# Performance work log

Measured on AMD Instinct MI355X. Metric: run time of the kernel, lower is better.

Reference implementation:

```python
import jax, jax.numpy as jnp
import numpy as np

# --- dims (match init_kwargs) ---
H = 2048      # hidden_dim
NH = 16       # num_heads
QL = 1536     # q_latent_dim
KVL = 512     # kv_latent_dim
QR = 64       # q_rope_dim (== k_rope_dim)
QN = 128      # q_nope_dim
KR = 64       # k_rope_dim
KN = 128      # k_nope_dim
VD = 128      # v_dim
B, S = 1, 2048
BASE = 10000.0
EPS = 1e-6


def rms_norm(x, w, eps=EPS):
    xf = x.astype(jnp.float32)
    var = jnp.mean(xf * xf, axis=-1, keepdims=True)
    return w * (xf * jax.lax.rsqrt(var + eps)).astype(x.dtype)


def rope_cos_sin(seq_len, dim, base=BASE):
    inv_freq = 1.0 / (base ** (jnp.arange(0, dim, 2, dtype=jnp.float32) / dim))
    t = jnp.arange(seq_len, dtype=jnp.float32)
    freqs = jnp.outer(t, inv_freq)
    emb = jnp.concatenate([freqs, freqs], axis=-1)  # [S, dim]
    return jnp.cos(emb), jnp.sin(emb)


def rotate_half(x):
    d = x.shape[-1] // 2
    return jnp.concatenate([-x[..., d:], x[..., :d]], axis=-1)


def apply_rotary_pos_emb(q, k, cos, sin, position_ids):
    # cos/sin: [S, d]; position_ids: [B, S] -> [B, 1, S, d]
    cos = cos[position_ids][:, None]
    sin = sin[position_ids][:, None]

    def interleave(x):  # matches view(b,h,s,d//2,2).transpose(4,3).reshape
        b, h, s, d = x.shape
        return x.reshape(b, h, s, d // 2, 2).transpose(0, 1, 2, 4, 3).reshape(b, h, s, d)

    q = interleave(q)
    k = interleave(k)
    return q * cos + rotate_half(q) * sin, k * cos + rotate_half(k) * sin


def setup_inputs() -> dict:
    key = jax.random.key(0)
    ks = jax.random.split(key, 8)
    sc = 0.02
    hidden_states = jax.random.normal(ks[0], (B, S, H), dtype=jnp.float32)
    position_ids = jnp.broadcast_to(jnp.arange(S, dtype=jnp.int32), (B, S))
    attn_mask = jnp.tril(jnp.ones((S, S), dtype=jnp.int32))[None, None]  # causal, [1,1,S,S]
    return {
        "hidden_states": hidden_states,
        "position_ids": position_ids,
        "attn_mask": attn_mask,
        "q_down_w": jax.random.normal(ks[1], (QL, H), jnp.float32) * sc,
        "kv_down_w": jax.random.normal(ks[2], (KVL + KR, H), jnp.float32) * sc,
        "q_up_w": jax.random.normal(ks[3], (NH * (QN + QR), QL), jnp.float32) * sc,
        "k_up_w": jax.random.normal(ks[4], (NH * (KN + VD), KVL), jnp.float32) * sc,
        "o_w": jax.random.normal(ks[5], (H, NH * VD), jnp.float32) * sc,
        "q_norm_w": jnp.ones((QL,), jnp.float32),
        "kv_norm_w": jnp.ones((KVL + KR,), jnp.float32),
    }


def reference(hidden_states, position_ids, attn_mask, q_down_w, kv_down_w,
              q_up_w, k_up_w, o_w, q_norm_w, kv_norm_w):
    bsz, seq_len, _ = hidden_states.shape

    # --- query path: down-proj -> RMSNorm -> up-proj ---
    latent_cq = rms_norm(hidden_states @ q_down_w.T, q_norm_w)        # [B,S,QL]
    q = latent_cq @ q_up_w.T                                          # [B,S,NH*(QN+QR)]
    q = q.reshape(bsz, seq_len, NH, QN + QR).transpose(0, 2, 1, 3)    # [B,NH,S,QN+QR]
    q_nope, q_pe = q[..., :QN], q[..., QN:]

    # --- kv path: down-proj -> RMSNorm -> split latent / shared k_pe ---
    compressed_kv = rms_norm(hidden_states @ kv_down_w.T, kv_norm_w)  # [B,S,KVL+KR]
    latent_ckv, k_pe = compressed_kv[..., :KVL], compressed_kv[..., KVL:]
    kv = latent_ckv @ k_up_w.T                                        # [B,S,NH*(KN+VD)]
    kv = kv.reshape(bsz, seq_len, NH, KN + VD).transpose(0, 2, 1, 3)  # [B,NH,S,KN+VD]
    k_nope, value = kv[..., :KN], kv[..., KN:]

    # --- partial RoPE on rotary sub-dims ---
    cos, sin = rope_cos_sin(seq_len, QR)
    k_pe = k_pe[:, None]                                              # [B,1,S,KR] shared across heads
    q_rope, k_rope = apply_rotary_pos_emb(q_pe, k_pe, cos, sin, position_ids)
    k_rope = jnp.broadcast_to(k_rope, (bsz, NH, seq_len, KR))

    query = jnp.concatenate([q_rope, q_nope], axis=-1)                # [B,NH,S,QR+QN]
    key = jnp.concatenate([k_rope, k_nope], axis=-1)                  # [B,NH,S,KR+KN]

    # --- explicit attention (no 1/sqrt(d) scale, matching the source) ---
    attn_weights = jnp.einsum('bhqd,bhkd->bhqk', query, key)
    attn_weights = jnp.where(attn_mask == 0, -jnp.inf, attn_weights)
    attn_weights = jax.nn.softmax(attn_weights, axis=-1)
    attn_output = jnp.einsum('bhqk,bhkd->bhqd', attn_weights, value)
    attn_output = attn_output.transpose(0, 2, 1, 3).reshape(bsz, seq_len, NH * VD)
    attn_output = attn_output @ o_w.T                                 # [B,S,H]
    return attn_weights, attn_output
```

## Files before the change

### kernel.cpp

```cpp
#include <hip/hip_runtime.h>
#include <cstdint>
#include <cmath>

typedef _Float16 f16;
using f16x8 = __attribute__((ext_vector_type(8))) _Float16;
using f16x4 = __attribute__((ext_vector_type(4))) _Float16;
using f32x4 = __attribute__((ext_vector_type(4))) float;

#define NHEAD 16
#define SEQ   2048
#define KS    2
#define KSS   4
#define NEG_INF -3.0e38f

static __device__ __forceinline__ f32x4 mfma16(f16x8 a, f16x8 b, f32x4 c) {
    return __builtin_amdgcn_mfma_f32_16x16x32_f16(a, b, c, 0, 0, 0);
}

static __device__ __forceinline__ void gload16(const void* gp, void* lp) {
    __builtin_amdgcn_global_load_lds(
        (const __attribute__((address_space(1))) unsigned int*)gp,
        (__attribute__((address_space(3))) unsigned int*)lp, 16, 0, 0);
}

__global__ __launch_bounds__(256) void k_cvt_all(
    const float* __restrict__ hsrc, const float* __restrict__ qdw, const float* __restrict__ kvdw,
    const float* __restrict__ quw, const float* __restrict__ kuw, const float* __restrict__ ow,
    f16* __restrict__ h16, f16* __restrict__ dw16, f16* __restrict__ quw16,
    f16* __restrict__ kuw16, f16* __restrict__ ow16, float* __restrict__ cs)
{
    constexpr int C1 = 1048576;
    constexpr int C2 = C1 + 786432;
    constexpr int C3 = C2 + 327680;
    constexpr int C4 = C3 + 1179648;
    constexpr int C5 = C4 + 524288;
    constexpr int C6 = C5 + 1048576;
    int chunk = blockIdx.x * 256 + threadIdx.x;
    if (chunk >= C6) {
        int idx = chunk - C6;
        if (idx < 65536) {
            int t = idx >> 5, j = idx & 31;
            float invf = (float)pow(10000.0, -(double)j / 32.0);
            float ang  = (float)t * invf;
            cs[t * 64 + j]      = (float)cos((double)ang);
            cs[t * 64 + 32 + j] = (float)sin((double)ang);
        }
        return;
    }
    const float* src; f16* dst; int off; int nvalid;
    if (chunk < C1)      { src = hsrc; dst = h16;  off = chunk;      nvalid = 4194304; }
    else if (chunk < C2) { src = qdw;  dst = dw16; off = chunk - C1; nvalid = 3145728; }
    else if (chunk < C3) { src = kvdw; dst = dw16 + 3145728; off = chunk - C2; nvalid = 1179648; }
    else if (chunk < C4) { src = quw;  dst = quw16; off = chunk - C3; nvalid = 4718592; }
    else if (chunk < C5) { src = kuw;  dst = kuw16; off = chunk - C4; nvalid = 2097152; }
    else                 { src = ow;   dst = ow16;  off = chunk - C5; nvalid = 4194304; }
    int i = off * 4;
    f16x4 o;
#pragma unroll
    for (int k = 0; k < 4; k++) {
        int idx = i + k;
        float v = (idx < nvalid) ? src[idx] : 0.f;
        o[k] = (f16)v;
    }
    *(f16x4*)&dst[i] = o;
}

template <typename OutT, bool NT>
static __device__ __forceinline__ void gemm_body(const f16* __restrict__ A, const f16* __restrict__ B,
                                                 OutT* __restrict__ C, int K, int ldc,
                                                 int m0, int n0, int k0, int k1,
                                                 f16* __restrict__ lds)
{
    const int tid  = threadIdx.x;
    const int lane = tid & 63;
    const int wv   = tid >> 6;
    const int l15  = lane & 15;
    const int lg   = lane >> 4;
    const int wm   = (wv >> 1) * 64;
    const int wn   = (wv & 1) * 64;

    f32x4 acc[4][4] = {};

    f16* As = lds;
    f16* Bs = lds + 8192;

    const int srow = tid >> 3;
    const int g    = (tid & 7) ^ (srow & 7);
    const f16* ap = &A[(size_t)(m0 + srow) * K + g * 8];
    const f16* bp = &B[(size_t)(n0 + srow) * K + g * 8];
    const int ldst = wv * 512;

    for (int kt = k0; kt < k1; kt += 64) {
        __syncthreads();
#pragma unroll
        for (int p = 0; p < 4; p++) {
            gload16(ap + (size_t)(p * 32) * K + kt, As + p * 2048 + ldst);
            gload16(bp + (size_t)(p * 32) * K + kt, Bs + p * 2048 + ldst);
        }
        __syncthreads();
#pragma unroll
        for (int ki = 0; ki < 2; ki++) {
            f16x8 af[4], bf[4];
#pragma unroll
            for (int i = 0; i < 4; i++) {
                const int ar = wm + i * 16 + l15;
                af[i] = *(const f16x8*)&As[ar * 64 + (((ki * 4 + lg) ^ (ar & 7)) << 3)];
            }
#pragma unroll
            for (int i = 0; i < 4; i++) {
                const int br = wn + i * 16 + l15;
                bf[i] = *(const f16x8*)&Bs[br * 64 + (((ki * 4 + lg) ^ (br & 7)) << 3)];
            }
#pragma unroll
            for (int i = 0; i < 4; i++)
#pragma unroll
                for (int j = 0; j < 4; j++)
                    acc[i][j] = mfma16(af[i], bf[j], acc[i][j]);
        }
    }
#pragma unroll
    for (int i = 0; i < 4; i++) {
#pragma unroll
        for (int j = 0; j < 4; j++) {
            const int row = m0 + wm + i * 16 + lg * 4;
            const int col = n0 + wn + j * 16 + l15;
#pragma unroll
            for (int r = 0; r < 4; r++) {
                if constexpr (NT)
                    __builtin_nontemporal_store((OutT)acc[i][j][r], &C[(size_t)(row + r) * ldc + col]);
                else
                    C[(size_t)(row + r) * ldc + col] = (OutT)acc[i][j][r];
            }
        }
    }
}

template <typename OutT, bool NT, int SPLITK>
__global__ __launch_bounds__(256) void k_gemm(const f16* __restrict__ A, const f16* __restrict__ B,
                                              OutT* __restrict__ C, int K, int ldc, size_t zstride)
{
    __shared__ __align__(16) f16 lds[16384];
    const int ks   = (SPLITK > 1) ? (int)blockIdx.z : 0;
    const int ksub = K / SPLITK;
    gemm_body<OutT, NT>(A, B, C + (size_t)ks * zstride, K, ldc,
                        blockIdx.y * 128, blockIdx.x * 128, ks * ksub, ks * ksub + ksub, lds);
}

__global__ __launch_bounds__(256) void k_up_fused(const f16* __restrict__ cq, const f16* __restrict__ quw,
                                                  f16* __restrict__ q_all,
                                                  const f16* __restrict__ lat, const f16* __restrict__ kuw,
                                                  f16* __restrict__ kv_all)
{
    __shared__ __align__(16) f16 lds[16384];
    if (blockIdx.x < 24)
        gemm_body<f16, false>(cq, quw, q_all, 1536, 3072,
                              blockIdx.y * 128, blockIdx.x * 128, 0, 1536, lds);
    else
        gemm_body<f16, false>(lat, kuw, kv_all, 512, 4096,
                              blockIdx.y * 128, (blockIdx.x - 24) * 128, 0, 512, lds);
}

__global__ __launch_bounds__(256) void k_add2f(const float* __restrict__ p, float* __restrict__ out)
{
    size_t i = ((size_t)blockIdx.x * 256 + threadIdx.x) * 4;
    f32x4 a = *(const f32x4*)&p[i];
    f32x4 b = *(const f32x4*)&p[(size_t)2048 * 2048 + i];
    __builtin_nontemporal_store(a + b, (f32x4*)&out[i]);
}

__global__ __launch_bounds__(256) void k_rms_both(const float* __restrict__ P0, const float* __restrict__ P1,
                                                  const float* __restrict__ wq, const float* __restrict__ wkv,
                                                  f16* __restrict__ cq, f16* __restrict__ lat,
                                                  f16* __restrict__ kro, const float* __restrict__ cs)
{
    const int row = blockIdx.x, tid = threadIdx.x;
    const float* a = &P0[(size_t)row * 2176];
    const float* b = &P1[(size_t)row * 2176];
    float ssq = 0.f, ssk = 0.f;
    for (int c = tid; c < 1536; c += 256) { float v = a[c] + b[c]; ssq += v * v; }
    for (int c = 1536 + tid; c < 2112; c += 256) { float v = a[c] + b[c]; ssk += v * v; }
#pragma unroll
    for (int off = 32; off > 0; off >>= 1) {
        ssq += __shfl_xor(ssq, off);
        ssk += __shfl_xor(ssk, off);
    }
    __shared__ float part[4][2];
    if ((tid & 63) == 0) { part[tid >> 6][0] = ssq; part[tid >> 6][1] = ssk; }
    __syncthreads();
    float totq = part[0][0] + part[1][0] + part[2][0] + part[3][0];
    float totk = part[0][1] + part[1][1] + part[2][1] + part[3][1];
    float scq = 1.f / sqrtf(totq / 1536.f + 1e-6f);
    float sck = 1.f / sqrtf(totk / 576.f + 1e-6f);
    for (int c = tid; c < 1536; c += 256)
        cq[(size_t)row * 1536 + c] = (f16)(wq[c] * (a[c] + b[c]) * scq);
    for (int c = tid; c < 512; c += 256)
        lat[(size_t)row * 512 + c] = (f16)(wkv[c] * (a[1536 + c] + b[1536 + c]) * sck);
    if (tid < 32) {
        int j = tid;
        float va = wkv[512 + 2 * j] * (a[2048 + 2 * j] + b[2048 + 2 * j]) * sck;
        float vb = wkv[512 + 2 * j + 1] * (a[2048 + 2 * j + 1] + b[2048 + 2 * j + 1]) * sck;
        float cv = cs[row * 64 + j], sv = cs[row * 64 + 32 + j];
        kro[row * 64 + j]      = (f16)(va * cv - vb * sv);
        kro[row * 64 + 32 + j] = (f16)(vb * cv + va * sv);
    }
}

__global__ __launch_bounds__(256) void k_asm_all(const f16* __restrict__ q_all, const float* __restrict__ cs,
                                                 f16* __restrict__ Qf,
                                                 const f16* __restrict__ kv_all,
                                                 f16* __restrict__ Knope,
                                                 f16* __restrict__ Vt)
{
    __shared__ __align__(16) f16 Vs[128][136];
    const int tid = threadIdx.x;

    if (blockIdx.x < 3072) {
        const int gid = blockIdx.x * 256 + tid;
        const int p   = gid % 24;
        const int rowi = gid / 24;
        const int h = rowi >> 11, s = rowi & 2047;
        const f16* qrow = &q_all[(size_t)s * 3072 + h * 192];
        f16x8 o;
        if (p < 8) {
            const int pp = (p < 4) ? p : (p - 4);
            f16x8 la = *(const f16x8*)&qrow[128 + 16 * pp];
            f16x8 lb = *(const f16x8*)&qrow[136 + 16 * pp];
            const float* cb = &cs[s * 64 + 8 * pp];
#pragma unroll
            for (int e = 0; e < 8; e++) {
                float av = (float)((e < 4) ? la[2 * e] : lb[2 * e - 8]);
                float bv = (float)((e < 4) ? la[2 * e + 1] : lb[2 * e - 7]);
                float cv = cb[e], sv = cb[32 + e];
                o[e] = (f16)((p < 4) ? (av * cv - bv * sv) : (bv * cv + av * sv));
            }
        } else {
            o = *(const f16x8*)&qrow[8 * p - 64];
        }
        *(f16x8*)&Qf[((size_t)h * SEQ + s) * 192 + 8 * p] = o;
        return;
    }

    const int b  = blockIdx.x - 3072;
    const int s0 = (b & 15) * 128;
    const int h  = b >> 4;
#pragma unroll
    for (int i = 0; i < 16; i++) {
        const int c = tid + 256 * i;
        const int s_loc = c >> 5;
        const int g = c & 31;
        f16x8 v = *(const f16x8*)&kv_all[(size_t)(s0 + s_loc) * 4096 + h * 256 + g * 8];
        if (g < 16) {
            *(f16x8*)&Knope[((size_t)h * 2048 + s0 + s_loc) * 128 + g * 8] = v;
        } else {
            const int d0 = (g - 16) * 8;
#pragma unroll
            for (int k = 0; k < 8; k++) Vs[d0 + k][s_loc] = v[k];
        }
    }
    __syncthreads();
#pragma unroll
    for (int i = 0; i < 8; i++) {
        const int c = tid + 256 * i;
        const int d = c >> 4;
        const int gs = c & 15;
        f16x8 v = *(const f16x8*)&Vs[d][gs * 8];
        *(f16x8*)&Vt[((size_t)h * 128 + d) * 2048 + s0 + gs * 8] = v;
    }
}

__global__ __launch_bounds__(256) void k_stats(
    const f16* __restrict__ Qf, const f16* __restrict__ Krope, const f16* __restrict__ Knope,
    float* __restrict__ mlpart)
{
    const int h  = blockIdx.z;
    const int ks = blockIdx.y;
    const int qt = blockIdx.x;
    const int q0 = qt * 64;
    const int tid = threadIdx.x;
    const int lane = tid & 63;
    const int wv = tid >> 6;
    const int l15 = lane & 15;
    const int lg  = lane >> 4;
    const int rowb = q0 + wv * 16;

    __shared__ __align__(16) f16 Ks_[64][200];

    float m[4], l[4];
#pragma unroll
    for (int r = 0; r < 4; r++) { m[r] = NEG_INF; l[r] = 0.f; }

    if (ks <= qt) {
        f16x8 qf[6];
        {
            const f16* qbase = &Qf[((size_t)h * SEQ + rowb + l15) * 192];
#pragma unroll
            for (int kf = 0; kf < 6; kf++)
                qf[kf] = *(const f16x8*)&qbase[kf * 32 + lg * 8];
        }
        const int srow = tid >> 2;
        const int sp4  = tid & 3;
        const f32x4 vzero = {0.f, 0.f, 0.f, 0.f};

        for (int t = ks; t <= qt; t += KSS) {
            const int c0 = t * 64;
            __syncthreads();
#pragma unroll
            for (int i = 0; i < 6; i++) {
                const int p = sp4 + 4 * i;
                f16x8 v;
                if (p < 8) v = *(const f16x8*)&Krope[(size_t)(c0 + srow) * 64 + p * 8];
                else       v = *(const f16x8*)&Knope[((size_t)h * SEQ + c0 + srow) * 128 + (p - 8) * 8];
                *(f16x8*)&Ks_[srow][p * 8] = v;
            }
            __syncthreads();

            f32x4 s[4];
#pragma unroll
            for (int ni = 0; ni < 4; ni++) {
                s[ni] = vzero;
                const f16* kp = &Ks_[ni * 16 + l15][0];
#pragma unroll
                for (int kf = 0; kf < 6; kf++)
                    s[ni] = mfma16(qf[kf], *(const f16x8*)&kp[kf * 32 + lg * 8], s[ni]);
            }

            float vmax[4] = {NEG_INF, NEG_INF, NEG_INF, NEG_INF};
#pragma unroll
            for (int ni = 0; ni < 4; ni++) {
                const int col = c0 + ni * 16 + l15;
#pragma unroll
                for (int r = 0; r < 4; r++) {
                    const int row = rowb + lg * 4 + r;
                    float v = (col <= row) ? s[ni][r] : NEG_INF;
                    s[ni][r] = v;
                    vmax[r] = fmaxf(vmax[r], v);
                }
            }
#pragma unroll
            for (int off = 1; off < 16; off <<= 1)
#pragma unroll
                for (int r = 0; r < 4; r++)
                    vmax[r] = fmaxf(vmax[r], __shfl_xor(vmax[r], off));
#pragma unroll
            for (int r = 0; r < 4; r++) {
                const float nm = fmaxf(m[r], vmax[r]);
                float es = 0.f;
#pragma unroll
                for (int ni = 0; ni < 4; ni++) es += expf(s[ni][r] - nm);
#pragma unroll
                for (int off = 1; off < 16; off <<= 1) es += __shfl_xor(es, off);
                l[r] = l[r] * expf(m[r] - nm) + es;
                m[r] = nm;
            }
        }
    }

    if (l15 == 0) {
#pragma unroll
        for (int r = 0; r < 4; r++) {
            const int rin = wv * 16 + lg * 4 + r;
            float* mp = &mlpart[((((size_t)h * 32 + qt) * KSS + ks) * 64 + rin) * 2];
            mp[0] = m[r];
            mp[1] = l[r];
        }
    }
}

__global__ __launch_bounds__(256) void k_pv(
    const f16* __restrict__ Qf, const f16* __restrict__ Krope, const f16* __restrict__ Knope,
    const f16* __restrict__ Vt, const float* __restrict__ mlpart,
    float* __restrict__ attnw,
    f16* __restrict__ Opart)
{
    const int h  = blockIdx.z;
    const int ks = blockIdx.y;
    const int qt = blockIdx.x;
    const int q0 = qt * 64;
    const int tid = threadIdx.x;
    const int lane = tid & 63;
    const int wv = tid >> 6;
    const int l15 = lane & 15;
    const int lg  = lane >> 4;
    const int rowb = q0 + wv * 16;

    __shared__ __align__(16) f16 Ks_[64][200];
    __shared__ __align__(16) f16 Vs[128][72];
    __shared__ __align__(16) f16 Plds[4][16][72];

    f16x8 qf[6];
    {
        const f16* qbase = &Qf[((size_t)h * SEQ + rowb + l15) * 192];
#pragma unroll
        for (int kf = 0; kf < 6; kf++)
            qf[kf] = *(const f16x8*)&qbase[kf * 32 + lg * 8];
    }

    float mr[4], rlr[4];
    {
        const float* base = &mlpart[(((size_t)h * 32 + qt) * KSS) * 64 * 2];
#pragma unroll
        for (int r = 0; r < 4; r++) {
            const int rin = wv * 16 + lg * 4 + r;
            float mm = NEG_INF, mk[KSS], lk[KSS];
#pragma unroll
            for (int k2 = 0; k2 < KSS; k2++) {
                mk[k2] = base[(k2 * 64 + rin) * 2];
                lk[k2] = base[(k2 * 64 + rin) * 2 + 1];
                mm = fmaxf(mm, mk[k2]);
            }
            float ll = 0.f;
#pragma unroll
            for (int k2 = 0; k2 < KSS; k2++) ll += lk[k2] * expf(mk[k2] - mm);
            mr[r]  = mm;
            rlr[r] = 1.f / ll;
        }
    }

    f32x4 o[8] = {};
    const f32x4 vzero = {0.f, 0.f, 0.f, 0.f};
    const int srow = tid >> 2;
    const int sp4  = tid & 3;

    for (int t = ks; t <= qt; t += KS) {
        const int c0 = t * 64;
        __syncthreads();
#pragma unroll
        for (int i = 0; i < 6; i++) {
            const int p = sp4 + 4 * i;
            f16x8 v;
            if (p < 8) v = *(const f16x8*)&Krope[(size_t)(c0 + srow) * 64 + p * 8];
            else       v = *(const f16x8*)&Knope[((size_t)h * SEQ + c0 + srow) * 128 + (p - 8) * 8];
            *(f16x8*)&Ks_[srow][p * 8] = v;
        }
#pragma unroll
        for (int i = 0; i < 4; i++) {
            const int c = tid + 256 * i;
            const int d = c >> 3, x = c & 7;
            *(f16x8*)&Vs[d][x * 8] = *(const f16x8*)&Vt[((size_t)h * 128 + d) * SEQ + c0 + x * 8];
        }
        __syncthreads();

        f32x4 s[4];
#pragma unroll
        for (int ni = 0; ni < 4; ni++) {
            s[ni] = vzero;
            const f16* kp = &Ks_[ni * 16 + l15][0];
#pragma unroll
            for (int kf = 0; kf < 6; kf++)
                s[ni] = mfma16(qf[kf], *(const f16x8*)&kp[kf * 32 + lg * 8], s[ni]);
        }

#pragma unroll
        for (int ni = 0; ni < 4; ni++) {
            const int col = c0 + ni * 16 + l15;
#pragma unroll
            for (int r = 0; r < 4; r++) {
                const int row = rowb + lg * 4 + r;
                float p = (col <= row) ? expf(s[ni][r] - mr[r]) * rlr[r] : 0.f;
                __builtin_nontemporal_store(p, &attnw[((size_t)h * SEQ + row) * SEQ + col]);
                Plds[wv][lg * 4 + r][ni * 16 + l15] = (f16)p;
            }
        }
        asm volatile("" ::: "memory");

        f16x8 pa0 = *(const f16x8*)&Plds[wv][l15][lg * 8];
        f16x8 pa1 = *(const f16x8*)&Plds[wv][l15][32 + lg * 8];
#pragma unroll
        for (int nd = 0; nd < 8; nd++) {
            const f16* vp = &Vs[nd * 16 + l15][lg * 8];
            o[nd] = mfma16(pa0, *(const f16x8*)&vp[0],  o[nd]);
            o[nd] = mfma16(pa1, *(const f16x8*)&vp[32], o[nd]);
        }
    }

#pragma unroll
    for (int nd = 0; nd < 8; nd++)
#pragma unroll
        for (int r = 0; r < 4; r++) {
            const int row = rowb + lg * 4 + r;
            Opart[((size_t)ks * SEQ + row) * 2048 + h * 128 + nd * 16 + l15] = (f16)o[nd][r];
        }

    if (ks == KS - 1) {
        const int cstart = q0 + 64;
        const int zc = SEQ - cstart;
        if (zc > 0) {
            const int nchunk = zc >> 2;
            for (int i = tid; i < 64 * nchunk; i += 256) {
                const int r  = i / nchunk;
                const int cc = (i - r * nchunk) << 2;
                __builtin_nontemporal_store(vzero,
                    (f32x4*)&attnw[((size_t)h * SEQ + q0 + r) * SEQ + cstart + cc]);
            }
        }
    }
}

__global__ __launch_bounds__(256) void k_ocomb(const f16* __restrict__ Opart, f16* __restrict__ Ohead)
{
    size_t i = ((size_t)blockIdx.x * 256 + threadIdx.x) * 8;
    f16x8 a = *(const f16x8*)&Opart[i];
    f16x8 b = *(const f16x8*)&Opart[(size_t)SEQ * 2048 + i];
    f16x8 o;
#pragma unroll
    for (int k = 0; k < 8; k++) o[k] = (f16)((float)a[k] + (float)b[k]);
    *(f16x8*)&Ohead[i] = o;
}

extern "C" void kernel_launch(void* const* d_in, const int* in_sizes, int n_in,
                              void* d_out, int out_size, void* d_ws, size_t ws_size,
                              hipStream_t stream)
{
    (void)in_sizes; (void)n_in; (void)out_size; (void)ws_size;
    const float* hidden    = (const float*)d_in[0];
    const float* q_down_w  = (const float*)d_in[3];
    const float* kv_down_w = (const float*)d_in[4];
    const float* q_up_w    = (const float*)d_in[5];
    const float* k_up_w    = (const float*)d_in[6];
    const float* o_w       = (const float*)d_in[7];
    const float* q_norm_w  = (const float*)d_in[8];
    const float* kv_norm_w = (const float*)d_in[9];

    float* attnw = (float*)d_out;
    float* outp  = attnw + (size_t)NHEAD * SEQ * SEQ;

    char* wp = (char*)d_ws;
    auto aws = [&](size_t bytes) { void* p = (void*)wp; wp += (bytes + 255) & ~(size_t)255; return p; };
    f16*  ow16  = (f16*)aws((size_t)2048 * 2048 * 2);
    f16*  Ohead = (f16*)aws((size_t)2048 * 2048 * 2);
    f16*  Qf    = (f16*)aws((size_t)16 * 2048 * 192 * 2);
    f16*  Knope = (f16*)aws((size_t)16 * 2048 * 128 * 2);
    f16*  Vt    = (f16*)aws((size_t)16 * 128 * 2048 * 2);
    f16*  Krope = (f16*)aws((size_t)2048 * 64 * 2);
    float* cs   = (float*)aws((size_t)2048 * 64 * 4);
    float* mlpart = (float*)aws((size_t)16 * 32 * KSS * 64 * 2 * 4);
    f16*  Opart   = (f16*)aws((size_t)KS * 2048 * 2048 * 2);
    float* opp    = (float*)Qf;

    char* sp = (char*)d_out;
    auto aso = [&](size_t bytes) { void* p = (void*)sp; sp += (bytes + 255) & ~(size_t)255; return p; };
    f16*  h16      = (f16*)aso((size_t)2048 * 2048 * 2);
    f16*  dw16     = (f16*)aso((size_t)2176 * 2048 * 2);
    f16*  quw16    = (f16*)aso((size_t)3072 * 1536 * 2);
    f16*  kuw16    = (f16*)aso((size_t)4096 * 512 * 2);
    float* down_part = (float*)aso((size_t)2 * 2048 * 2176 * 4);
    f16*  cq16     = (f16*)aso((size_t)2048 * 1536 * 2);
    f16*  latent16 = (f16*)aso((size_t)2048 * 512 * 2);
    f16*  q_all    = (f16*)aso((size_t)2048 * 3072 * 2);
    f16*  kv_all   = (f16*)aso((size_t)2048 * 4096 * 2);

    k_cvt_all<<<dim3(19456), dim3(256), 0, stream>>>(
        hidden, q_down_w, kv_down_w, q_up_w, k_up_w, o_w,
        h16, dw16, quw16, kuw16, ow16, cs);

    k_gemm<float, false, 2><<<dim3(17, 16, 2), dim3(256), 0, stream>>>(
        h16, dw16, down_part, 2048, 2176, (size_t)2048 * 2176);

    k_rms_both<<<dim3(2048), dim3(256), 0, stream>>>(
        down_part, down_part + (size_t)2048 * 2176, q_norm_w, kv_norm_w,
        cq16, latent16, Krope, cs);

    k_up_fused<<<dim3(56, 16), dim3(256), 0, stream>>>(cq16, quw16, q_all, latent16, kuw16, kv_all);

    k_asm_all<<<dim3(3072 + 256), dim3(256), 0, stream>>>(q_all, cs, Qf, kv_all, Knope, Vt);

    k_stats<<<dim3(32, KSS, 16), dim3(256), 0, stream>>>(Qf, Krope, Knope, mlpart);
    k_pv<<<dim3(32, KS, 16), dim3(256), 0, stream>>>(Qf, Krope, Knope, Vt, mlpart, attnw, Opart);
    k_ocomb<<<dim3(2048), dim3(256), 0, stream>>>(Opart, Ohead);

    k_gemm<float, false, 2><<<dim3(16, 16, 2), dim3(256), 0, stream>>>(
        Ohead, ow16, opp, 2048, 2048, (size_t)2048 * 2048);
    k_add2f<<<dim3(4096), dim3(256), 0, stream>>>(opp, outp);
}
```

Measured before the change: 376.7 us.

## Use 128-row query tiles with 512-thread blocks in attention kernels

The stats and PV attention kernels now handle 128 query rows per block with 8 waves instead of 64 rows with 4 waves. Each staged K/V tile in shared memory is therefore reused by twice as many query rows. Heads 8 and up process query tiles in reverse order to even out causal load across blocks. Waves whose rows lie entirely above a key tile skip the compute, and in PV they write zeros to those attention-weight entries. The cost is fewer blocks in the grid and some waves idling on diagonal tiles.

```diff
diff --git a/kernel.cpp b/kernel.cpp
--- a/kernel.cpp
+++ b/kernel.cpp
@@ -268,14 +268,14 @@
     }
 }
 
-__global__ __launch_bounds__(256) void k_stats(
+__global__ __launch_bounds__(512) void k_stats(
     const f16* __restrict__ Qf, const f16* __restrict__ Krope, const f16* __restrict__ Knope,
     float* __restrict__ mlpart)
 {
     const int h  = blockIdx.z;
     const int ks = blockIdx.y;
-    const int qt = blockIdx.x;
-    const int q0 = qt * 64;
+    const int qt = (h >= 8) ? (15 - (int)blockIdx.x) : (int)blockIdx.x;
+    const int q0 = qt * 128;
     const int tid = threadIdx.x;
     const int lane = tid & 63;
     const int wv = tid >> 6;
@@ -289,7 +289,8 @@
 #pragma unroll
     for (int r = 0; r < 4; r++) { m[r] = NEG_INF; l[r] = 0.f; }
 
-    if (ks <= qt) {
+    const int ntiles = 2 * qt + 2;
+    if (ks < ntiles) {
         f16x8 qf[6];
         {
             const f16* qbase = &Qf[((size_t)h * SEQ + rowb + l15) * 192];
@@ -297,22 +298,24 @@
             for (int kf = 0; kf < 6; kf++)
                 qf[kf] = *(const f16x8*)&qbase[kf * 32 + lg * 8];
         }
-        const int srow = tid >> 2;
-        const int sp4  = tid & 3;
+        const int srow = tid >> 3;
+        const int sp8  = tid & 7;
         const f32x4 vzero = {0.f, 0.f, 0.f, 0.f};
 
-        for (int t = ks; t <= qt; t += KSS) {
+        for (int t = ks; t < ntiles; t += KSS) {
             const int c0 = t * 64;
             __syncthreads();
 #pragma unroll
-            for (int i = 0; i < 6; i++) {
-                const int p = sp4 + 4 * i;
+            for (int i = 0; i < 3; i++) {
+                const int p = sp8 + 8 * i;
                 f16x8 v;
                 if (p < 8) v = *(const f16x8*)&Krope[(size_t)(c0 + srow) * 64 + p * 8];
                 else       v = *(const f16x8*)&Knope[((size_t)h * SEQ + c0 + srow) * 128 + (p - 8) * 8];
                 *(f16x8*)&Ks_[srow][p * 8] = v;
             }
             __syncthreads();
+
+            if (rowb + 15 < c0) continue;
 
             f32x4 s[4];
 #pragma unroll
@@ -359,14 +362,14 @@
 #pragma unroll
         for (int r = 0; r < 4; r++) {
             const int rin = wv * 16 + lg * 4 + r;
-            float* mp = &mlpart[((((size_t)h * 32 + qt) * KSS + ks) * 64 + rin) * 2];
+            float* mp = &mlpart[((((size_t)h * 16 + qt) * KSS + ks) * 128 + rin) * 2];
             mp[0] = m[r];
             mp[1] = l[r];
         }
     }
 }
 
-__global__ __launch_bounds__(256) void k_pv(
+__global__ __launch_bounds__(512) void k_pv(
     const f16* __restrict__ Qf, const f16* __restrict__ Krope, const f16* __restrict__ Knope,
     const f16* __restrict__ Vt, const float* __restrict__ mlpart,
     float* __restrict__ attnw,
@@ -374,8 +377,8 @@
 {
     const int h  = blockIdx.z;
     const int ks = blockIdx.y;
-    const int qt = blockIdx.x;
-    const int q0 = qt * 64;
+    const int qt = (h >= 8) ? (15 - (int)blockIdx.x) : (int)blockIdx.x;
+    const int q0 = qt * 128;
     const int tid = threadIdx.x;
     const int lane = tid & 63;
     const int wv = tid >> 6;
@@ -385,7 +388,7 @@
 
     __shared__ __align__(16) f16 Ks_[64][200];
     __shared__ __align__(16) f16 Vs[128][72];
-    __shared__ __align__(16) f16 Plds[4][16][72];
+    __shared__ __align__(16) f16 Plds[8][16][72];
 
     f16x8 qf[6];
     {
@@ -397,15 +400,15 @@
 
     float mr[4], rlr[4];
     {
-        const float* base = &mlpart[(((size_t)h * 32 + qt) * KSS) * 64 * 2];
+        const float* base = &mlpart[(((size_t)h * 16 + qt) * KSS) * 128 * 2];
 #pragma unroll
         for (int r = 0; r < 4; r++) {
             const int rin = wv * 16 + lg * 4 + r;
             float mm = NEG_INF, mk[KSS], lk[KSS];
 #pragma unroll
             for (int k2 = 0; k2 < KSS; k2++) {
-                mk[k2] = base[(k2 * 64 + rin) * 2];
-                lk[k2] = base[(k2 * 64 + rin) * 2 + 1];
+                mk[k2] = base[(k2 * 128 + rin) * 2];
+                lk[k2] = base[(k2 * 128 + rin) * 2 + 1];
                 mm = fmaxf(mm, mk[k2]);
             }
             float ll = 0.f;
@@ -418,27 +421,41 @@
 
     f32x4 o[8] = {};
     const f32x4 vzero = {0.f, 0.f, 0.f, 0.f};
-    const int srow = tid >> 2;
-    const int sp4  = tid & 3;
-
-    for (int t = ks; t <= qt; t += KS) {
+    const int srow = tid >> 3;
+    const int sp8  = tid & 7;
+    const int ntiles = 2 * qt + 2;
+
+    for (int t = ks; t < ntiles; t += KS) {
         const int c0 = t * 64;
         __syncthreads();
 #pragma unroll
-        for (int i = 0; i < 6; i++) {
-            const int p = sp4 + 4 * i;
+        for (int i = 0; i < 3; i++) {
+            const int p = sp8 + 8 * i;
             f16x8 v;
             if (p < 8) v = *(const f16x8*)&Krope[(size_t)(c0 + srow) * 64 + p * 8];
             else       v = *(const f16x8*)&Knope[((size_t)h * SEQ + c0 + srow) * 128 + (p - 8) * 8];
             *(f16x8*)&Ks_[srow][p * 8] = v;
         }
 #pragma unroll
-        for (int i = 0; i < 4; i++) {
-            const int c = tid + 256 * i;
+        for (int i = 0; i < 2; i++) {
+            const int c = tid + 512 * i;
             const int d = c >> 3, x = c & 7;
             *(f16x8*)&Vs[d][x * 8] = *(const f16x8*)&Vt[((size_t)h * 128 + d) * SEQ + c0 + x * 8];
         }
         __syncthreads();
+
+        if (rowb + 15 < c0) {
+#pragma unroll
+            for (int ni = 0; ni < 4; ni++) {
+                const int col = c0 + ni * 16 + l15;
+#pragma unroll
+                for (int r = 0; r < 4; r++) {
+                    const int row = rowb + lg * 4 + r;
+                    __builtin_nontemporal_store(0.f, &attnw[((size_t)h * SEQ + row) * SEQ + col]);
+                }
+            }
+            continue;
+        }
 
         f32x4 s[4];
 #pragma unroll
@@ -482,11 +499,11 @@
         }
 
     if (ks == KS - 1) {
-        const int cstart = q0 + 64;
+        const int cstart = q0 + 128;
         const int zc = SEQ - cstart;
         if (zc > 0) {
             const int nchunk = zc >> 2;
-            for (int i = tid; i < 64 * nchunk; i += 256) {
+            for (int i = tid; i < 128 * nchunk; i += 512) {
                 const int r  = i / nchunk;
                 const int cc = (i - r * nchunk) << 2;
                 __builtin_nontemporal_store(vzero,
@@ -533,7 +550,7 @@
     f16*  Vt    = (f16*)aws((size_t)16 * 128 * 2048 * 2);
     f16*  Krope = (f16*)aws((size_t)2048 * 64 * 2);
     float* cs   = (float*)aws((size_t)2048 * 64 * 4);
-    float* mlpart = (float*)aws((size_t)16 * 32 * KSS * 64 * 2 * 4);
+    float* mlpart = (float*)aws((size_t)16 * 16 * KSS * 128 * 2 * 4);
     f16*  Opart   = (f16*)aws((size_t)KS * 2048 * 2048 * 2);
     float* opp    = (float*)Qf;
 
@@ -564,8 +581,8 @@
 
     k_asm_all<<<dim3(3072 + 256), dim3(256), 0, stream>>>(q_all, cs, Qf, kv_all, Knope, Vt);
 
-    k_stats<<<dim3(32, KSS, 16), dim3(256), 0, stream>>>(Qf, Krope, Knope, mlpart);
-    k_pv<<<dim3(32, KS, 16), dim3(256), 0, stream>>>(Qf, Krope, Knope, Vt, mlpart, attnw, Opart);
+    k_stats<<<dim3(16, KSS, 16), dim3(512), 0, stream>>>(Qf, Krope, Knope, mlpart);
+    k_pv<<<dim3(16, KS, 16), dim3(512), 0, stream>>>(Qf, Krope, Knope, Vt, mlpart, attnw, Opart);
     k_ocomb<<<dim3(2048), dim3(256), 0, stream>>>(Opart, Ohead);
 
     k_gemm<float, false, 2><<<dim3(16, 16, 2), dim3(256), 0, stream>>>(
```

New measurement: 382.0 us. Within noise of the previous version (+1.4%).
